# Kernel tuning notes

Hardware: AMD Instinct MI355X
Metric: run time of the kernel (lower is better)

Reference implementation:

```python
import jax, jax.numpy as jnp
import numpy as np

B = 16384      # batch
T = 14         # number of embedding tables
L = 100000     # rows per table (table has L+1 rows due to the +1 offset)
E = 16         # em_size
H = 50         # user click history length


def setup_inputs() -> dict:
    key = jax.random.key(0)
    ks = jax.random.split(key, 10)
    sparse_features = jax.random.randint(ks[0], (B, T), 0, L, dtype=jnp.int32)
    dense_features = jax.random.normal(ks[1], (B, 1), dtype=jnp.float32)
    user_click_history = jax.random.randint(ks[2], (B, H), 0, L, dtype=jnp.int32)
    # stacked EmbeddingBag weights: [T, L+1, E]
    W = jax.random.normal(ks[3], (T, L + 1, E), dtype=jnp.float32) * 0.01
    fc1_w = jax.random.normal(ks[4], (200, 241), dtype=jnp.float32) / np.sqrt(241).astype(np.float32)
    fc1_b = jnp.zeros((200,), jnp.float32)
    fc2_w = jax.random.normal(ks[5], (80, 200), dtype=jnp.float32) / np.sqrt(200).astype(np.float32)
    fc2_b = jnp.zeros((80,), jnp.float32)
    fc3_w = jax.random.normal(ks[6], (2, 80), dtype=jnp.float32) / np.sqrt(80).astype(np.float32)
    fc3_b = jnp.zeros((2,), jnp.float32)
    return dict(sparse_features=sparse_features, dense_features=dense_features,
                user_click_history=user_click_history, W=W,
                fc1_w=fc1_w, fc1_b=fc1_b, fc2_w=fc2_w, fc2_b=fc2_b,
                fc3_w=fc3_w, fc3_b=fc3_b)


def reference(sparse_features, dense_features, user_click_history, W,
              fc1_w, fc1_b, fc2_w, fc2_b, fc3_w, fc3_b):
    # Per-table single-index EmbeddingBag(sum) == plain lookup. Batched gather
    # across all T tables at once: [B, T, E]
    embs = W[jnp.arange(T)[None, :], sparse_features + 1]
    embs = embs.reshape(embs.shape[0], T * E)  # [B, T*E]
    # tables[0].weight row 0 is zeroed before the history lookup (padding row).
    W0 = W[0].at[0].set(0.0)
    hist = W0[user_click_history + 1].sum(axis=1)  # [B, E] EmbeddingBag sum
    x = jnp.concatenate([embs, hist, dense_features], axis=1)  # [B, 241]
    x = jax.nn.relu(x @ fc1_w.T + fc1_b)
    x = jax.nn.relu(x @ fc2_w.T + fc2_b)
    return x @ fc3_w.T + fc3_b  # [B, 2]
```

## Files before the change

### kernel.cpp

```cpp
#include <hip/hip_runtime.h>


using u16 = unsigned short;
typedef __attribute__((ext_vector_type(8))) short short8v;
typedef __attribute__((ext_vector_type(4))) short short4v;
typedef __attribute__((ext_vector_type(4))) float floatx4;

constexpr int W1_ELEMS = 13 * 8 * 64 * 8;
constexpr int W2_ELEMS = 5 * 7 * 64 * 8;
constexpr int EF_ELEMS = 1024 * 7 * 64 * 8;

__device__ __forceinline__ u16 f2bf(float f) {
  unsigned u = __float_as_uint(f);
  unsigned r = (u + 0x7fffu + ((u >> 16) & 1u)) >> 16;
  return (u16)r;
}
__device__ __forceinline__ float bf2f(u16 h) {
  return __uint_as_float(((unsigned)h) << 16);
}

__global__ __launch_bounds__(256) void prep_kernel(
    const float* __restrict__ w1, const float* __restrict__ w2,
    const float* __restrict__ W, const int* __restrict__ sf,
    const int* __restrict__ hist, const float* __restrict__ dense,
    u16* __restrict__ w1h, u16* __restrict__ w2h,
    u16* __restrict__ ef, u16* __restrict__ hs) {
  const int b = blockIdx.x;
  const int tix = threadIdx.x;
  short8v z8 = {0, 0, 0, 0, 0, 0, 0, 0};

  if (b < 35) {
    int tid = b * 256 + tix;
    if (tid < 13 * 8 * 64) {
      int l = tid & 63;
      int g = tid >> 6;
      int kt = g & 7, nt = g >> 3;
      int n = nt * 16 + (l & 15);
      int kb = kt * 32 + (l >> 4) * 8;
      short8v h8;
#pragma unroll
      for (int e = 0; e < 8; ++e) {
        int k = kb + e;
        float v = (n < 200 && k < 241) ? w1[n * 241 + k] : 0.f;
        h8[e] = (short)f2bf(v);
      }
      *(short8v*)&w1h[tid * 8] = h8;
    } else if (tid < 13 * 8 * 64 + 5 * 7 * 64) {
      int t2 = tid - 13 * 8 * 64;
      int l = t2 & 63;
      int g = t2 >> 6;
      int kt = g % 7, nt = g / 7;
      int n = nt * 16 + (l & 15);
      int kb = kt * 32 + (l >> 4) * 8;
      short8v h8;
#pragma unroll
      for (int e = 0; e < 8; ++e) {
        int k = kb + e;
        float v = (k < 200) ? w2[n * 200 + k] : 0.f;
        h8[e] = (short)f2bf(v);
      }
      *(short8v*)&w2h[t2 * 8] = h8;
    }
  } else if (b < 3619) {
    int g = (b - 35) * 256 + tix;
    int t = g >> 16;
    int bb = (g >> 2) & 16383;
    int q = g & 3;
    int idx = sf[bb * 14 + t] + 1;
    floatx4 v4 = *(const floatx4*)(W + ((size_t)t * 100001 + (size_t)idx) * 16 + q * 4);
    short4v h4;
#pragma unroll
    for (int d = 0; d < 4; ++d) h4[d] = (short)f2bf(v4[d]);
    int k0 = t * 16 + q * 4;
    int kt = k0 >> 5, kg = (k0 >> 3) & 3, e0 = k0 & 7;
    int tile = bb >> 4, r = bb & 15;
    *(short4v*)&ef[((tile * 7 + kt) * 64 + kg * 16 + r) * 8 + e0] = h4;
  } else {
    int tile = b - 3619;
    int row0 = tile * 16;
    int r = tix >> 4, rem = tix & 15, q = rem & 3, s = rem >> 2;
    const int* hp = hist + (row0 + r) * 50;
    float a0 = 0.f, a1 = 0.f, a2 = 0.f, a3 = 0.f;
#pragma unroll
    for (int hh = 0; hh < 12; ++hh) {
      int idx = hp[s + hh * 4] + 1;
      floatx4 p = *(const floatx4*)(W + (size_t)idx * 16 + q * 4);
      a0 += p[0];
      a1 += p[1];
      a2 += p[2];
      a3 += p[3];
    }
    if (s < 2) {
      int idx = hp[48 + s] + 1;
      floatx4 p = *(const floatx4*)(W + (size_t)idx * 16 + q * 4);
      a0 += p[0];
      a1 += p[1];
      a2 += p[2];
      a3 += p[3];
    }
    a0 += __shfl_xor(a0, 4);
    a1 += __shfl_xor(a1, 4);
    a2 += __shfl_xor(a2, 4);
    a3 += __shfl_xor(a3, 4);
    a0 += __shfl_xor(a0, 8);
    a1 += __shfl_xor(a1, 8);
    a2 += __shfl_xor(a2, 8);
    a3 += __shfl_xor(a3, 8);
    if (s == 0) {
      float vals[4] = {a0, a1, a2, a3};
      short4v h4, l4;
#pragma unroll
      for (int d = 0; d < 4; ++d) {
        u16 hi = f2bf(vals[d]);
        h4[d] = (short)hi;
        l4[d] = (short)f2bf(vals[d] - bf2f(hi));
      }
      u16* ht = hs + (size_t)tile * 1024;
      int base = ((q >> 1) * 16 + r) * 8 + ((q * 4) & 7);
      *(short4v*)&ht[base] = h4;
      *(short4v*)&ht[512 + base] = l4;
      if (q == 0) {
        float dv = dense[row0 + r];
        u16 dh = f2bf(dv), dl = f2bf(dv - bf2f(dh));
        short8v dh8 = z8, dl8 = z8;
        dh8[0] = (short)dh;
        dl8[0] = (short)dl;
        *(short8v*)&ht[(32 + r) * 8] = dh8;
        *(short8v*)&ht[512 + (32 + r) * 8] = dl8;
        *(short8v*)&ht[(48 + r) * 8] = z8;
        *(short8v*)&ht[512 + (48 + r) * 8] = z8;
      }
    }
  }
}

__global__ __launch_bounds__(1024, 4) void mlp_kernel(
    const u16* __restrict__ ef, const u16* __restrict__ hs,
    const u16* __restrict__ w1h, const u16* __restrict__ w2h,
    const float* __restrict__ b1, const float* __restrict__ b2,
    const float* __restrict__ w3, const float* __restrict__ b3,
    float* __restrict__ out) {
  __shared__ u16 A2h[4 * 7 * 64 * 8], A2l[4 * 7 * 64 * 8];
  __shared__ float o2[64 * 84];

  const int tid = threadIdx.x;
  const int l = tid & 63;
  const int w = tid >> 6;
  const int sub = w & 3;
  const int ntg = w >> 2;
  const int blk = blockIdx.x;
  const int tile = blk * 4 + sub;
  const int row0 = blk * 64;
  short8v z8 = {0, 0, 0, 0, 0, 0, 0, 0};
  const int ntbase = (ntg == 0) ? 0 : 4 + 3 * (ntg - 1);
  const int ntcnt = (ntg == 0) ? 4 : 3;

  const u16* ht = hs + (size_t)tile * 1024;
  short8v a7h = *(const short8v*)&ht[l * 8];
  short8v a7l = *(const short8v*)&ht[512 + l * 8];

  short8v ga[2];
  ga[0] = *(const short8v*)&ef[((tile * 7 + 0) * 64 + l) * 8];
  ga[1] = *(const short8v*)&ef[((tile * 7 + 1) * 64 + l) * 8];

  short8v bhr[2][4];
#pragma unroll
  for (int kk = 0; kk < 2; ++kk)
#pragma unroll
    for (int i = 0; i < 4; ++i)
      bhr[kk][i] = (i < ntcnt) ? *(const short8v*)&w1h[(((ntbase + i) * 8 + kk) * 64 + l) * 8]
                               : z8;

  floatx4 acc[4];
#pragma unroll
  for (int i = 0; i < 4; ++i) acc[i] = (floatx4){0.f, 0.f, 0.f, 0.f};

#pragma unroll
  for (int kt = 0; kt < 8; ++kt) {
    const int cur = kt & 1;
    short8v ah = (kt < 7) ? ga[cur] : a7h;
    if (kt < 5) ga[cur] = *(const short8v*)&ef[((tile * 7 + kt + 2) * 64 + l) * 8];
#pragma unroll
    for (int i = 0; i < 4; ++i) {
      if (i < ntcnt) {
        short8v cb = bhr[cur][i];
        if (kt < 6)
          bhr[cur][i] = *(const short8v*)&w1h[(((ntbase + i) * 8 + kt + 2) * 64 + l) * 8];
        acc[i] = __builtin_amdgcn_mfma_f32_16x16x32_bf16(ah, cb, acc[i], 0, 0, 0);
        if (kt == 7)
          acc[i] = __builtin_amdgcn_mfma_f32_16x16x32_bf16(a7l, cb, acc[i], 0, 0, 0);
      }
    }
    if (kt == 2 || kt == 5) __builtin_amdgcn_s_barrier();
  }

  const bool dual = (ntg == 3);
  short8v bra[2], brb[2];
  bra[0] = *(const short8v*)&w2h[((ntg * 7 + 0) * 64 + l) * 8];
  bra[1] = *(const short8v*)&w2h[((ntg * 7 + 1) * 64 + l) * 8];
  brb[0] = dual ? *(const short8v*)&w2h[((4 * 7 + 0) * 64 + l) * 8] : z8;
  brb[1] = dual ? *(const short8v*)&w2h[((4 * 7 + 1) * 64 + l) * 8] : z8;

#pragma unroll
  for (int i = 0; i < 4; ++i) {
    if (i < ntcnt) {
      int n = (ntbase + i) * 16 + (l & 15);
      float bias = (n < 200) ? b1[n] : 0.f;
      int kt2 = n >> 5, kg2 = (n >> 3) & 3, e = n & 7;
#pragma unroll
      for (int g = 0; g < 4; ++g) {
        float v = (n < 200) ? fmaxf(acc[i][g] + bias, 0.f) : 0.f;
        int m = (l >> 4) * 4 + g;
        u16 hi = f2bf(v), lo = f2bf(v - bf2f(hi));
        int pos = ((sub * 7 + kt2) * 64 + kg2 * 16 + m) * 8 + e;
        A2h[pos] = hi;
        A2l[pos] = lo;
      }
    }
  }
  if (ntg == 1 && l < 32) {
    *(short8v*)&A2h[((sub * 7 + 6) * 64 + 32 + l) * 8] = z8;
    *(short8v*)&A2l[((sub * 7 + 6) * 64 + 32 + l) * 8] = z8;
  }
  __syncthreads();

  floatx4 acc2a = (floatx4){0.f, 0.f, 0.f, 0.f};
  floatx4 acc2b = (floatx4){0.f, 0.f, 0.f, 0.f};
#pragma unroll
  for (int kt = 0; kt < 7; ++kt) {
    short8v ah = *(const short8v*)&A2h[((sub * 7 + kt) * 64 + l) * 8];
    short8v al = *(const short8v*)&A2l[((sub * 7 + kt) * 64 + l) * 8];
    short8v ca = bra[kt & 1];
    if (kt < 5) bra[kt & 1] = *(const short8v*)&w2h[((ntg * 7 + kt + 2) * 64 + l) * 8];
    acc2a = __builtin_amdgcn_mfma_f32_16x16x32_bf16(ah, ca, acc2a, 0, 0, 0);
    acc2a = __builtin_amdgcn_mfma_f32_16x16x32_bf16(al, ca, acc2a, 0, 0, 0);
    if (dual) {
      short8v cb2 = brb[kt & 1];
      if (kt < 5) brb[kt & 1] = *(const short8v*)&w2h[((4 * 7 + kt + 2) * 64 + l) * 8];
      acc2b = __builtin_amdgcn_mfma_f32_16x16x32_bf16(ah, cb2, acc2b, 0, 0, 0);
      acc2b = __builtin_amdgcn_mfma_f32_16x16x32_bf16(al, cb2, acc2b, 0, 0, 0);
    }
  }

  {
    int n = ntg * 16 + (l & 15);
    float bias = b2[n];
#pragma unroll
    for (int g = 0; g < 4; ++g) {
      int r2 = sub * 16 + (l >> 4) * 4 + g;
      o2[r2 * 84 + n] = fmaxf(acc2a[g] + bias, 0.f);
    }
    if (dual) {
      int n2 = 64 + (l & 15);
      float bias2 = b2[n2];
#pragma unroll
      for (int g = 0; g < 4; ++g) {
        int r2 = sub * 16 + (l >> 4) * 4 + g;
        o2[r2 * 84 + n2] = fmaxf(acc2b[g] + bias2, 0.f);
      }
    }
  }
  __syncthreads();

  if (tid < 128) {
    int r = tid >> 1, o = tid & 1;
    float a = b3[o];
    const float* orow = &o2[r * 84];
    const float* wrow = &w3[o * 80];
#pragma unroll
    for (int j = 0; j < 80; j += 4) {
      floatx4 xv = *(const floatx4*)&orow[j];
      floatx4 wv4 = *(const floatx4*)&wrow[j];
      a += xv[0] * wv4[0] + xv[1] * wv4[1] + xv[2] * wv4[2] + xv[3] * wv4[3];
    }
    out[(row0 + r) * 2 + o] = a;
  }
}

extern "C" void kernel_launch(void* const* d_in, const int* in_sizes, int n_in,
                              void* d_out, int out_size, void* d_ws, size_t ws_size,
                              hipStream_t stream) {
  const int* sf = (const int*)d_in[0];
  const float* dense = (const float*)d_in[1];
  const int* hist = (const int*)d_in[2];
  const float* W = (const float*)d_in[3];
  const float* w1 = (const float*)d_in[4];
  const float* b1 = (const float*)d_in[5];
  const float* w2 = (const float*)d_in[6];
  const float* b2 = (const float*)d_in[7];
  const float* w3 = (const float*)d_in[8];
  const float* b3 = (const float*)d_in[9];
  float* out = (float*)d_out;

  u16* w1h = (u16*)d_ws;
  u16* w2h = w1h + W1_ELEMS;
  u16* ef = w2h + W2_ELEMS;
  u16* hs = ef + EF_ELEMS;

  prep_kernel<<<dim3(35 + 3584 + 1024), dim3(256), 0, stream>>>(
      w1, w2, W, sf, hist, dense, w1h, w2h, ef, hs);
  mlp_kernel<<<dim3(256), dim3(1024), 0, stream>>>(ef, hs, w1h, w2h, b1, b2, w3, b3, out);
}
```

Measured before the change: 35.26 us.

## Shrink MLP blocks to one 16-row tile and preload all operands into registers

The MLP kernel now launches 1024 blocks of 256 threads, each handling one 16-row tile, instead of 256 blocks of 1024 threads handling four tiles. The double-buffered software prefetch of activations and weights is replaced by loading every A and B fragment for both layers into registers up front, and the intra-loop s_barrier calls are removed. The goal is more independent blocks to hide latency and fewer barriers, at the cost of much higher register pressure. That pressure could lower occupancy or cause spills.

```diff
diff --git a/kernel.cpp b/kernel.cpp
--- a/kernel.cpp
+++ b/kernel.cpp
@@ -134,23 +134,20 @@
   }
 }
 
-__global__ __launch_bounds__(1024, 4) void mlp_kernel(
+__global__ __launch_bounds__(256, 2) void mlp_kernel(
     const u16* __restrict__ ef, const u16* __restrict__ hs,
     const u16* __restrict__ w1h, const u16* __restrict__ w2h,
     const float* __restrict__ b1, const float* __restrict__ b2,
     const float* __restrict__ w3, const float* __restrict__ b3,
     float* __restrict__ out) {
-  __shared__ u16 A2h[4 * 7 * 64 * 8], A2l[4 * 7 * 64 * 8];
-  __shared__ float o2[64 * 84];
+  __shared__ u16 A2h[7 * 64 * 8], A2l[7 * 64 * 8];
+  __shared__ float o2[16 * 84];
 
   const int tid = threadIdx.x;
   const int l = tid & 63;
-  const int w = tid >> 6;
-  const int sub = w & 3;
-  const int ntg = w >> 2;
-  const int blk = blockIdx.x;
-  const int tile = blk * 4 + sub;
-  const int row0 = blk * 64;
+  const int ntg = tid >> 6;
+  const int tile = blockIdx.x;
+  const int row0 = tile * 16;
   short8v z8 = {0, 0, 0, 0, 0, 0, 0, 0};
   const int ntbase = (ntg == 0) ? 0 : 4 + 3 * (ntg - 1);
   const int ntcnt = (ntg == 0) ? 4 : 3;
@@ -158,18 +155,22 @@
   const u16* ht = hs + (size_t)tile * 1024;
   short8v a7h = *(const short8v*)&ht[l * 8];
   short8v a7l = *(const short8v*)&ht[512 + l * 8];
-
-  short8v ga[2];
-  ga[0] = *(const short8v*)&ef[((tile * 7 + 0) * 64 + l) * 8];
-  ga[1] = *(const short8v*)&ef[((tile * 7 + 1) * 64 + l) * 8];
-
-  short8v bhr[2][4];
-#pragma unroll
-  for (int kk = 0; kk < 2; ++kk)
-#pragma unroll
-    for (int i = 0; i < 4; ++i)
-      bhr[kk][i] = (i < ntcnt) ? *(const short8v*)&w1h[(((ntbase + i) * 8 + kk) * 64 + l) * 8]
-                               : z8;
+  short8v ga[7];
+#pragma unroll
+  for (int kt = 0; kt < 7; ++kt)
+    ga[kt] = *(const short8v*)&ef[((tile * 7 + kt) * 64 + l) * 8];
+
+  short8v b1r[4][8];
+#pragma unroll
+  for (int i = 0; i < 4; ++i) {
+#pragma unroll
+    for (int kt = 0; kt < 8; ++kt) {
+      if (i < ntcnt)
+        b1r[i][kt] = *(const short8v*)&w1h[(((ntbase + i) * 8 + kt) * 64 + l) * 8];
+      else
+        b1r[i][kt] = z8;
+    }
+  }
 
   floatx4 acc[4];
 #pragma unroll
@@ -177,29 +178,24 @@
 
 #pragma unroll
   for (int kt = 0; kt < 8; ++kt) {
-    const int cur = kt & 1;
-    short8v ah = (kt < 7) ? ga[cur] : a7h;
-    if (kt < 5) ga[cur] = *(const short8v*)&ef[((tile * 7 + kt + 2) * 64 + l) * 8];
+    short8v ah = (kt < 7) ? ga[kt] : a7h;
 #pragma unroll
     for (int i = 0; i < 4; ++i) {
       if (i < ntcnt) {
-        short8v cb = bhr[cur][i];
-        if (kt < 6)
-          bhr[cur][i] = *(const short8v*)&w1h[(((ntbase + i) * 8 + kt + 2) * 64 + l) * 8];
-        acc[i] = __builtin_amdgcn_mfma_f32_16x16x32_bf16(ah, cb, acc[i], 0, 0, 0);
+        acc[i] = __builtin_amdgcn_mfma_f32_16x16x32_bf16(ah, b1r[i][kt], acc[i], 0, 0, 0);
         if (kt == 7)
-          acc[i] = __builtin_amdgcn_mfma_f32_16x16x32_bf16(a7l, cb, acc[i], 0, 0, 0);
-      }
-    }
-    if (kt == 2 || kt == 5) __builtin_amdgcn_s_barrier();
+          acc[i] = __builtin_amdgcn_mfma_f32_16x16x32_bf16(a7l, b1r[i][kt], acc[i], 0, 0, 0);
+      }
+    }
   }
 
   const bool dual = (ntg == 3);
-  short8v bra[2], brb[2];
-  bra[0] = *(const short8v*)&w2h[((ntg * 7 + 0) * 64 + l) * 8];
-  bra[1] = *(const short8v*)&w2h[((ntg * 7 + 1) * 64 + l) * 8];
-  brb[0] = dual ? *(const short8v*)&w2h[((4 * 7 + 0) * 64 + l) * 8] : z8;
-  brb[1] = dual ? *(const short8v*)&w2h[((4 * 7 + 1) * 64 + l) * 8] : z8;
+  short8v b2a[7], b2b[7];
+#pragma unroll
+  for (int kt = 0; kt < 7; ++kt) {
+    b2a[kt] = *(const short8v*)&w2h[((ntg * 7 + kt) * 64 + l) * 8];
+    b2b[kt] = dual ? *(const short8v*)&w2h[((4 * 7 + kt) * 64 + l) * 8] : z8;
+  }
 
 #pragma unroll
   for (int i = 0; i < 4; ++i) {
@@ -212,15 +208,15 @@
         float v = (n < 200) ? fmaxf(acc[i][g] + bias, 0.f) : 0.f;
         int m = (l >> 4) * 4 + g;
         u16 hi = f2bf(v), lo = f2bf(v - bf2f(hi));
-        int pos = ((sub * 7 + kt2) * 64 + kg2 * 16 + m) * 8 + e;
+        int pos = (kt2 * 64 + kg2 * 16 + m) * 8 + e;
         A2h[pos] = hi;
         A2l[pos] = lo;
       }
     }
   }
   if (ntg == 1 && l < 32) {
-    *(short8v*)&A2h[((sub * 7 + 6) * 64 + 32 + l) * 8] = z8;
-    *(short8v*)&A2l[((sub * 7 + 6) * 64 + 32 + l) * 8] = z8;
+    *(short8v*)&A2h[(6 * 64 + 32 + l) * 8] = z8;
+    *(short8v*)&A2l[(6 * 64 + 32 + l) * 8] = z8;
   }
   __syncthreads();
 
@@ -228,17 +224,13 @@
   floatx4 acc2b = (floatx4){0.f, 0.f, 0.f, 0.f};
 #pragma unroll
   for (int kt = 0; kt < 7; ++kt) {
-    short8v ah = *(const short8v*)&A2h[((sub * 7 + kt) * 64 + l) * 8];
-    short8v al = *(const short8v*)&A2l[((sub * 7 + kt) * 64 + l) * 8];
-    short8v ca = bra[kt & 1];
-    if (kt < 5) bra[kt & 1] = *(const short8v*)&w2h[((ntg * 7 + kt + 2) * 64 + l) * 8];
-    acc2a = __builtin_amdgcn_mfma_f32_16x16x32_bf16(ah, ca, acc2a, 0, 0, 0);
-    acc2a = __builtin_amdgcn_mfma_f32_16x16x32_bf16(al, ca, acc2a, 0, 0, 0);
+    short8v ah = *(const short8v*)&A2h[(kt * 64 + l) * 8];
+    short8v al = *(const short8v*)&A2l[(kt * 64 + l) * 8];
+    acc2a = __builtin_amdgcn_mfma_f32_16x16x32_bf16(ah, b2a[kt], acc2a, 0, 0, 0);
+    acc2a = __builtin_amdgcn_mfma_f32_16x16x32_bf16(al, b2a[kt], acc2a, 0, 0, 0);
     if (dual) {
-      short8v cb2 = brb[kt & 1];
-      if (kt < 5) brb[kt & 1] = *(const short8v*)&w2h[((4 * 7 + kt + 2) * 64 + l) * 8];
-      acc2b = __builtin_amdgcn_mfma_f32_16x16x32_bf16(ah, cb2, acc2b, 0, 0, 0);
-      acc2b = __builtin_amdgcn_mfma_f32_16x16x32_bf16(al, cb2, acc2b, 0, 0, 0);
+      acc2b = __builtin_amdgcn_mfma_f32_16x16x32_bf16(ah, b2b[kt], acc2b, 0, 0, 0);
+      acc2b = __builtin_amdgcn_mfma_f32_16x16x32_bf16(al, b2b[kt], acc2b, 0, 0, 0);
     }
   }
 
@@ -247,7 +239,7 @@
     float bias = b2[n];
 #pragma unroll
     for (int g = 0; g < 4; ++g) {
-      int r2 = sub * 16 + (l >> 4) * 4 + g;
+      int r2 = (l >> 4) * 4 + g;
       o2[r2 * 84 + n] = fmaxf(acc2a[g] + bias, 0.f);
     }
     if (dual) {
@@ -255,14 +247,14 @@
       float bias2 = b2[n2];
 #pragma unroll
       for (int g = 0; g < 4; ++g) {
-        int r2 = sub * 16 + (l >> 4) * 4 + g;
+        int r2 = (l >> 4) * 4 + g;
         o2[r2 * 84 + n2] = fmaxf(acc2b[g] + bias2, 0.f);
       }
     }
   }
   __syncthreads();
 
-  if (tid < 128) {
+  if (tid < 32) {
     int r = tid >> 1, o = tid & 1;
     float a = b3[o];
     const float* orow = &o2[r * 84];
@@ -299,5 +291,5 @@
 
   prep_kernel<<<dim3(35 + 3584 + 1024), dim3(256), 0, stream>>>(
       w1, w2, W, sf, hist, dense, w1h, w2h, ef, hs);
-  mlp_kernel<<<dim3(256), dim3(1024), 0, stream>>>(ef, hs, w1h, w2h, b1, b2, w3, b3, out);
-}
+  mlp_kernel<<<dim3(1024), dim3(256), 0, stream>>>(ef, hs, w1h, w2h, b1, b2, w3, b3, out);
+}
```

Result: slower. 36.95 us (+4.8%).
